# Kernel tuning notes

Measured on AMD Instinct MI355X. Metric: run time of the kernel, lower is better.

Reference implementation:

```python
import jax, jax.numpy as jnp
from jax import lax
import numpy as np

# dims
N = 8192        # words in sentence
LMAX = 16       # max chars per word (padded)
WED = 506       # word embedding dim
WHD = 512       # word LSTM hidden (input = WED + CHD = 512)
CED = 6         # char embedding dim
CHD = 6         # char LSTM hidden (hardcoded 6 in original)
WV = 50000      # word vocab
CV = 128        # char vocab
T = 64          # tagset size


def setup_inputs() -> dict:
    key = jax.random.key(0)
    ks = jax.random.split(key, 14)
    s = 0.1
    nrm = lambda k, shp: (jax.random.normal(k, shp, dtype=jnp.float32) * s)
    return {
        "sentence_words": jax.random.randint(ks[0], (N,), 0, WV),
        "sentence_characters": jax.random.randint(ks[1], (N, LMAX), 0, CV),
        "char_lengths": jax.random.randint(ks[2], (N,), 1, LMAX + 1),
        "word_emb": nrm(ks[3], (WV, WED)),
        "char_emb": nrm(ks[4], (CV, CED)),
        # PyTorch LSTM gate order: i, f, g, o. b = b_ih + b_hh combined.
        "c_Wih": nrm(ks[5], (4 * CHD, CED)),
        "c_Whh": nrm(ks[6], (4 * CHD, CHD)),
        "c_b": nrm(ks[7], (4 * CHD,)),
        "w_Wih": nrm(ks[8], (4 * WHD, WED + CHD)),
        "w_Whh": nrm(ks[9], (4 * WHD, WHD)),
        "w_b": nrm(ks[10], (4 * WHD,)),
        "out_W": nrm(ks[11], (T, WHD)),
        "out_b": nrm(ks[12], (T,)),
    }


def _gates(pre, c_prev):
    i, f, g, o = jnp.split(pre, 4, axis=-1)
    i = jax.nn.sigmoid(i)
    f = jax.nn.sigmoid(f)
    g = jnp.tanh(g)
    o = jax.nn.sigmoid(o)
    c_new = f * c_prev + i * g
    h_new = o * jnp.tanh(c_new)
    return h_new, c_new


def reference(sentence_words, sentence_characters, char_lengths,
              word_emb, char_emb, c_Wih, c_Whh, c_b,
              w_Wih, w_Whh, w_b, out_W, out_b):
    # ---- char-level LSTM: all words batched, masked by length ----
    ce = char_emb[sentence_characters]                  # [N, LMAX, CED]
    xproj = jnp.einsum('nlc,gc->nlg', ce, c_Wih) + c_b  # [N, LMAX, 4*CHD]
    xproj_t = jnp.swapaxes(xproj, 0, 1)                 # [LMAX, N, 4*CHD]
    mask_t = (jnp.arange(LMAX)[:, None] < char_lengths[None, :])[..., None]  # [LMAX, N, 1]

    def char_step(carry, xm):
        h, c = carry
        xp, m = xm
        h_new, c_new = _gates(xp + h @ c_Whh.T, c)
        return (jnp.where(m, h_new, h), jnp.where(m, c_new, c)), None

    z = jnp.zeros((N, CHD), dtype=xproj.dtype)
    (h_char, _), _ = lax.scan(char_step, (z, z), (xproj_t, mask_t))  # [N, CHD]

    # ---- word-level LSTM over the sentence (batch = 1) ----
    we = word_emb[sentence_words]                       # [N, WED]
    x = jnp.concatenate([we, h_char], axis=1)           # [N, WED+CHD]
    xp = x @ w_Wih.T + w_b                              # [N, 4*WHD]

    def word_step(carry, xt):
        h, c = carry
        h_new, c_new = _gates(xt + h @ w_Whh.T, c)
        return (h_new, c_new), h_new

    zw = jnp.zeros((WHD,), dtype=xp.dtype)
    _, hs = lax.scan(word_step, (zw, zw), xp)           # [N, WHD]

    logits = hs @ out_W.T + out_b                       # [N, T]
    return jax.nn.log_softmax(logits, axis=1)
```

## Files before the change

### kernel.cpp

```cpp
#include <hip/hip_runtime.h>
#include <hip/hip_bf16.h>
#include <math.h>

#define N_WORDS 8192
#define LMAX    16
#define WED     506
#define WHD     512
#define CED     6
#define CHD     6
#define CVOC    128
#define TAG     64
#define XDIM    512
#define G4      2048
#define NWG     64

__device__ __forceinline__ float fast_sigmoid(float x) { return 1.0f / (1.0f + __expf(-x)); }
__device__ __forceinline__ float fast_tanh(float x)    { return 2.0f / (1.0f + __expf(-2.0f * x)) - 1.0f; }

__global__ void __launch_bounds__(256) char_lstm_kernel(
    const int*   __restrict__ chars,
    const int*   __restrict__ lens,
    const float* __restrict__ char_emb,
    const float* __restrict__ cWih,
    const float* __restrict__ cWhh,
    const float* __restrict__ cb,
    float*       __restrict__ h_char)
{
    __shared__ float sWih[24][6], sWhh[24][6], sb[24], semb[CVOC][CED];
    int t = threadIdx.x;
    if (t < 144) { sWih[t / 6][t % 6] = cWih[t]; sWhh[t / 6][t % 6] = cWhh[t]; }
    if (t < 24) sb[t] = cb[t];
    for (int i = t; i < CVOC * CED; i += 256) semb[i / CED][i % CED] = char_emb[i];
    __syncthreads();

    int n = blockIdx.x * 256 + t;
    if (n >= N_WORDS) return;
    int len = lens[n];
    float h[CHD] = {0, 0, 0, 0, 0, 0};
    float c[CHD] = {0, 0, 0, 0, 0, 0};
    for (int l = 0; l < LMAX; ++l) {
        if (l >= len) break;
        int ch = chars[n * LMAX + l];
        float e[CED];
        #pragma unroll
        for (int k = 0; k < CED; ++k) e[k] = semb[ch][k];
        float pre[24];
        #pragma unroll
        for (int g = 0; g < 24; ++g) {
            float a = sb[g];
            #pragma unroll
            for (int k = 0; k < CED; ++k) a += e[k] * sWih[g][k];
            #pragma unroll
            for (int k = 0; k < CHD; ++k) a += h[k] * sWhh[g][k];
            pre[g] = a;
        }
        #pragma unroll
        for (int u = 0; u < CHD; ++u) {
            float ig = fast_sigmoid(pre[u]);
            float fg = fast_sigmoid(pre[6 + u]);
            float gg = fast_tanh(pre[12 + u]);
            float og = fast_sigmoid(pre[18 + u]);
            float cn = fg * c[u] + ig * gg;
            c[u] = cn;
            h[u] = og * fast_tanh(cn);
        }
    }
    for (int u = 0; u < CHD; ++u) h_char[n * CHD + u] = h[u];
}

__global__ void __launch_bounds__(256) build_x_kernel(
    const int*   __restrict__ words,
    const float* __restrict__ word_emb,
    const float* __restrict__ h_char,
    float*       __restrict__ X)
{
    long idx = (long)blockIdx.x * 256 + threadIdx.x;
    if (idx >= (long)N_WORDS * XDIM) return;
    int n = (int)(idx >> 9), k = (int)(idx & 511);
    float v;
    if (k < WED) v = word_emb[(long)words[n] * WED + k];
    else         v = h_char[n * CHD + (k - WED)];
    X[idx] = v;
}

#define BM 64
#define BN 64
#define BK 16
__global__ void __launch_bounds__(256) xp_gemm_kernel(
    const float* __restrict__ X,
    const float* __restrict__ Wih,
    const float* __restrict__ wb,
    float*       __restrict__ XP4)
{
    __shared__ float As[BM][BK + 1];
    __shared__ float Bs[BN][BK + 1];
    int tid = threadIdx.x;
    int bm = (blockIdx.x % (N_WORDS / BM)) * BM;
    int bn = (blockIdx.x / (N_WORDS / BM)) * BN;
    int ty = tid / 16, tx = tid % 16;
    float acc[4][4] = {};
    for (int k0 = 0; k0 < XDIM; k0 += BK) {
        #pragma unroll
        for (int i = 0; i < 4; ++i) {
            int e = tid + i * 256;
            int r = e >> 4, cc = e & 15;
            As[r][cc] = X[(long)(bm + r) * XDIM + k0 + cc];
            Bs[r][cc] = Wih[(long)(bn + r) * XDIM + k0 + cc];
        }
        __syncthreads();
        #pragma unroll
        for (int kk = 0; kk < BK; ++kk) {
            float a[4], b[4];
            #pragma unroll
            for (int i = 0; i < 4; ++i) a[i] = As[ty * 4 + i][kk];
            #pragma unroll
            for (int j = 0; j < 4; ++j) b[j] = Bs[tx * 4 + j][kk];
            #pragma unroll
            for (int i = 0; i < 4; ++i)
                #pragma unroll
                for (int j = 0; j < 4; ++j) acc[i][j] += a[i] * b[j];
        }
        __syncthreads();
    }
    #pragma unroll
    for (int i = 0; i < 4; ++i) {
        int m = bm + ty * 4 + i;
        #pragma unroll
        for (int j = 0; j < 4; ++j) {
            int g = bn + tx * 4 + j;
            int unit = g & 511, gate = g >> 9;
            XP4[((long)m * WHD + unit) * 4 + gate] = acc[i][j] + wb[g];
        }
    }
}

__global__ void __launch_bounds__(256, 1) word_lstm_kernel(
    const float* __restrict__ Whh,
    const float* __restrict__ XP4,
    float*       HS)
{
    __shared__ float hbuf[WHD];

    const int tid = threadIdx.x;
    const int wg  = blockIdx.x;
    const int ug  = tid >> 5;
    const int p   = tid & 31;
    const int j   = wg * 8 + ug;

    float w[4][16];
    #pragma unroll
    for (int r = 0; r < 4; ++r) {
        const float* src = Whh + (long)(r * 512 + j) * WHD + p;
        #pragma unroll
        for (int kk = 0; kk < 16; ++kk) w[r][kk] = src[kk * 32];
    }

    float c = 0.0f;
    float h16[16];
    #pragma unroll
    for (int kk = 0; kk < 16; ++kk) h16[kk] = 0.0f;

    for (int t = 0; t < N_WORDS; ++t) {
        const float4 xp = *(const float4*)(XP4 + ((long)t * WHD + j) * 4);

        if (t > 0) {
            if (tid < 64) {
                const unsigned long long* hrow =
                    (const unsigned long long*)(HS + (long)(t - 1) * WHD);
                float lo[4], hi[4];
                bool ready = false;
                while (!ready) {
                    unsigned long long q[4];
                    #pragma unroll
                    for (int i = 0; i < 4; ++i)
                        q[i] = __hip_atomic_load(&hrow[i * 64 + tid], __ATOMIC_RELAXED,
                                                 __HIP_MEMORY_SCOPE_AGENT);
                    ready = true;
                    #pragma unroll
                    for (int i = 0; i < 4; ++i) {
                        lo[i] = __uint_as_float((unsigned)(q[i] & 0xffffffffu));
                        hi[i] = __uint_as_float((unsigned)(q[i] >> 32));
                        ready = ready && (lo[i] > 0.5f) && (hi[i] > 0.5f);
                    }
                }
                #pragma unroll
                for (int i = 0; i < 4; ++i) {
                    hbuf[i * 128 + 2 * tid]     = lo[i] - 2.0f;
                    hbuf[i * 128 + 2 * tid + 1] = hi[i] - 2.0f;
                }
            }
            __syncthreads();
            #pragma unroll
            for (int kk = 0; kk < 16; ++kk) h16[kk] = hbuf[p + 32 * kk];
        }

        float di = 0, df = 0, dg = 0, dq = 0;
        #pragma unroll
        for (int kk = 0; kk < 16; ++kk) {
            di = fmaf(w[0][kk], h16[kk], di);
            df = fmaf(w[1][kk], h16[kk], df);
            dg = fmaf(w[2][kk], h16[kk], dg);
            dq = fmaf(w[3][kk], h16[kk], dq);
        }
        #pragma unroll
        for (int m = 16; m >= 1; m >>= 1) {
            di += __shfl_xor(di, m);
            df += __shfl_xor(df, m);
            dg += __shfl_xor(dg, m);
            dq += __shfl_xor(dq, m);
        }
        float ig = fast_sigmoid(xp.x + di);
        float fg = fast_sigmoid(xp.y + df);
        float gg = fast_tanh(xp.z + dg);
        float og = fast_sigmoid(xp.w + dq);
        c = fg * c + ig * gg;
        float hn = og * fast_tanh(c);

        if (p == 0)
            __hip_atomic_store(&HS[(long)t * WHD + j], hn + 2.0f, __ATOMIC_RELAXED,
                               __HIP_MEMORY_SCOPE_AGENT);
    }
}

__global__ void __launch_bounds__(256) transpose_outw_kernel(
    const float* __restrict__ outW, float* __restrict__ outWT)
{
    int e = blockIdx.x * 256 + threadIdx.x;
    if (e >= TAG * WHD) return;
    int g = e >> 9, k = e & 511;
    outWT[k * TAG + g] = outW[e];
}

__global__ void __launch_bounds__(64) logits_kernel(
    const float* __restrict__ HS,
    const float* __restrict__ outWT,
    const float* __restrict__ outb,
    float*       __restrict__ out)
{
    int n = blockIdx.x;
    int g = threadIdx.x;
    const float* hrow = HS + (long)n * WHD;
    float acc = outb[g];
    #pragma unroll 8
    for (int k = 0; k < WHD; ++k) acc += (hrow[k] - 2.0f) * outWT[k * TAG + g];
    float m = acc;
    #pragma unroll
    for (int s = 32; s >= 1; s >>= 1) m = fmaxf(m, __shfl_xor(m, s));
    float ex = __expf(acc - m);
    float ssum = ex;
    #pragma unroll
    for (int s = 32; s >= 1; s >>= 1) ssum += __shfl_xor(ssum, s);
    out[(long)n * TAG + g] = acc - m - logf(ssum);
}

extern "C" void kernel_launch(void* const* d_in, const int* in_sizes, int n_in,
                              void* d_out, int out_size, void* d_ws, size_t ws_size,
                              hipStream_t stream)
{
    const int*   words = (const int*)   d_in[0];
    const int*   chars = (const int*)   d_in[1];
    const int*   lens  = (const int*)   d_in[2];
    const float* wemb  = (const float*) d_in[3];
    const float* cemb  = (const float*) d_in[4];
    const float* cWih  = (const float*) d_in[5];
    const float* cWhh  = (const float*) d_in[6];
    const float* cb    = (const float*) d_in[7];
    const float* wWih  = (const float*) d_in[8];
    const float* wWhh  = (const float*) d_in[9];
    const float* wb    = (const float*) d_in[10];
    const float* outW  = (const float*) d_in[11];
    const float* outb  = (const float*) d_in[12];
    float* out = (float*)d_out;

    char* ws = (char*)d_ws;
    size_t off = 0;
    float* h_char = (float*)(ws + off); off += (size_t)N_WORDS * CHD * 4;
    float* X      = (float*)(ws + off); off += (size_t)N_WORDS * XDIM * 4;
    float* XP4    = (float*)(ws + off); off += (size_t)N_WORDS * G4 * 4;
    float* HS     = (float*)(ws + off); off += (size_t)N_WORDS * WHD * 4;
    float* outWT  = (float*)(ws + off); off += (size_t)WHD * TAG * 4;

    hipMemsetAsync(HS, 0, (size_t)N_WORDS * WHD * sizeof(float), stream);

    char_lstm_kernel<<<N_WORDS / 256, 256, 0, stream>>>(chars, lens, cemb, cWih, cWhh, cb, h_char);
    build_x_kernel<<<(N_WORDS * XDIM) / 256, 256, 0, stream>>>(words, wemb, h_char, X);
    xp_gemm_kernel<<<(N_WORDS / BM) * (G4 / BN), 256, 0, stream>>>(X, wWih, wb, XP4);
    transpose_outw_kernel<<<(TAG * WHD) / 256, 256, 0, stream>>>(outW, outWT);
    word_lstm_kernel<<<NWG, 256, 0, stream>>>(wWhh, XP4, HS);
    logits_kernel<<<N_WORDS, 64, 0, stream>>>(HS, outWT, outb, out);
}
```

Before: 18.05 ms.

## Move recurrent weights to LDS as bf16 and poll h per chunk with backoff

The word LSTM kernel now holds each workgroup's slice of Whh in shared memory as packed bf16 instead of 64 fp32 registers per thread. Each step unpacks the weights from LDS before the dot products. The spin-wait on the previous hidden state now re-polls only the chunks not yet ready and sleeps briefly after repeated misses. This is meant to free registers and cut polling traffic on the serial critical path, at the cost of an extra LDS read each step and reduced weight precision.

```diff
diff --git a/kernel.cpp b/kernel.cpp
--- a/kernel.cpp
+++ b/kernel.cpp
@@ -139,21 +139,33 @@
     const float* __restrict__ XP4,
     float*       HS)
 {
+    __shared__ uint2 wlds[4 * 16 * 64];
     __shared__ float hbuf[WHD];
 
     const int tid = threadIdx.x;
     const int wg  = blockIdx.x;
+    const int v   = tid >> 6;
+    const int l   = tid & 63;
     const int ug  = tid >> 5;
     const int p   = tid & 31;
     const int j   = wg * 8 + ug;
 
-    float w[4][16];
-    #pragma unroll
-    for (int r = 0; r < 4; ++r) {
+    #pragma unroll
+    for (int s = 0; s < 16; ++s) {
+        int r  = s >> 2;
+        int kb = (s & 3) * 4;
         const float* src = Whh + (long)(r * 512 + j) * WHD + p;
-        #pragma unroll
-        for (int kk = 0; kk < 16; ++kk) w[r][kk] = src[kk * 32];
-    }
+        unsigned short b[4];
+        #pragma unroll
+        for (int i = 0; i < 4; ++i) {
+            __hip_bfloat16 hb = __float2bfloat16(src[(kb + i) * 32]);
+            b[i] = *(unsigned short*)&hb;
+        }
+        wlds[(v * 16 + s) * 64 + l] =
+            make_uint2((unsigned)b[0] | ((unsigned)b[1] << 16),
+                       (unsigned)b[2] | ((unsigned)b[3] << 16));
+    }
+    __syncthreads();
 
     float c = 0.0f;
     float h16[16];
@@ -168,20 +180,40 @@
                 const unsigned long long* hrow =
                     (const unsigned long long*)(HS + (long)(t - 1) * WHD);
                 float lo[4], hi[4];
-                bool ready = false;
-                while (!ready) {
-                    unsigned long long q[4];
-                    #pragma unroll
-                    for (int i = 0; i < 4; ++i)
-                        q[i] = __hip_atomic_load(&hrow[i * 64 + tid], __ATOMIC_RELAXED,
-                                                 __HIP_MEMORY_SCOPE_AGENT);
-                    ready = true;
-                    #pragma unroll
-                    for (int i = 0; i < 4; ++i) {
-                        lo[i] = __uint_as_float((unsigned)(q[i] & 0xffffffffu));
-                        hi[i] = __uint_as_float((unsigned)(q[i] >> 32));
-                        ready = ready && (lo[i] > 0.5f) && (hi[i] > 0.5f);
+                bool done0 = false, done1 = false, done2 = false, done3 = false;
+                int fails = 0;
+                for (;;) {
+                    unsigned long long q;
+                    if (!done0) {
+                        q = __hip_atomic_load(&hrow[0 * 64 + tid], __ATOMIC_RELAXED,
+                                              __HIP_MEMORY_SCOPE_AGENT);
+                        lo[0] = __uint_as_float((unsigned)(q & 0xffffffffu));
+                        hi[0] = __uint_as_float((unsigned)(q >> 32));
+                        done0 = (lo[0] > 0.5f) && (hi[0] > 0.5f);
                     }
+                    if (!done1) {
+                        q = __hip_atomic_load(&hrow[1 * 64 + tid], __ATOMIC_RELAXED,
+                                              __HIP_MEMORY_SCOPE_AGENT);
+                        lo[1] = __uint_as_float((unsigned)(q & 0xffffffffu));
+                        hi[1] = __uint_as_float((unsigned)(q >> 32));
+                        done1 = (lo[1] > 0.5f) && (hi[1] > 0.5f);
+                    }
+                    if (!done2) {
+                        q = __hip_atomic_load(&hrow[2 * 64 + tid], __ATOMIC_RELAXED,
+                                              __HIP_MEMORY_SCOPE_AGENT);
+                        lo[2] = __uint_as_float((unsigned)(q & 0xffffffffu));
+                        hi[2] = __uint_as_float((unsigned)(q >> 32));
+                        done2 = (lo[2] > 0.5f) && (hi[2] > 0.5f);
+                    }
+                    if (!done3) {
+                        q = __hip_atomic_load(&hrow[3 * 64 + tid], __ATOMIC_RELAXED,
+                                              __HIP_MEMORY_SCOPE_AGENT);
+                        lo[3] = __uint_as_float((unsigned)(q & 0xffffffffu));
+                        hi[3] = __uint_as_float((unsigned)(q >> 32));
+                        done3 = (lo[3] > 0.5f) && (hi[3] > 0.5f);
+                    }
+                    if (done0 && done1 && done2 && done3) break;
+                    if (++fails >= 3) __builtin_amdgcn_s_sleep(2);
                 }
                 #pragma unroll
                 for (int i = 0; i < 4; ++i) {
@@ -194,25 +226,32 @@
             for (int kk = 0; kk < 16; ++kk) h16[kk] = hbuf[p + 32 * kk];
         }
 
-        float di = 0, df = 0, dg = 0, dq = 0;
-        #pragma unroll
-        for (int kk = 0; kk < 16; ++kk) {
-            di = fmaf(w[0][kk], h16[kk], di);
-            df = fmaf(w[1][kk], h16[kk], df);
-            dg = fmaf(w[2][kk], h16[kk], dg);
-            dq = fmaf(w[3][kk], h16[kk], dq);
+        float acc[4] = {0.0f, 0.0f, 0.0f, 0.0f};
+        #pragma unroll
+        for (int s = 0; s < 16; ++s) {
+            uint2 qw = wlds[(v * 16 + s) * 64 + l];
+            int r  = s >> 2;
+            int kb = (s & 3) * 4;
+            float w0 = __uint_as_float(qw.x << 16);
+            float w1 = __uint_as_float(qw.x & 0xffff0000u);
+            float w2 = __uint_as_float(qw.y << 16);
+            float w3 = __uint_as_float(qw.y & 0xffff0000u);
+            acc[r] = fmaf(w0, h16[kb + 0], acc[r]);
+            acc[r] = fmaf(w1, h16[kb + 1], acc[r]);
+            acc[r] = fmaf(w2, h16[kb + 2], acc[r]);
+            acc[r] = fmaf(w3, h16[kb + 3], acc[r]);
         }
         #pragma unroll
         for (int m = 16; m >= 1; m >>= 1) {
-            di += __shfl_xor(di, m);
-            df += __shfl_xor(df, m);
-            dg += __shfl_xor(dg, m);
-            dq += __shfl_xor(dq, m);
-        }
-        float ig = fast_sigmoid(xp.x + di);
-        float fg = fast_sigmoid(xp.y + df);
-        float gg = fast_tanh(xp.z + dg);
-        float og = fast_sigmoid(xp.w + dq);
+            acc[0] += __shfl_xor(acc[0], m);
+            acc[1] += __shfl_xor(acc[1], m);
+            acc[2] += __shfl_xor(acc[2], m);
+            acc[3] += __shfl_xor(acc[3], m);
+        }
+        float ig = fast_sigmoid(xp.x + acc[0]);
+        float fg = fast_sigmoid(xp.y + acc[1]);
+        float gg = fast_tanh(xp.z + acc[2]);
+        float og = fast_sigmoid(xp.w + acc[3]);
         c = fg * c + ig * gg;
         float hn = og * fast_tanh(c);
 
```

New measurement: 23.03 ms (median of 2 runs). 27.6% more time.
